# Performance work log

Measured on AMD Instinct MI355X. Metric: run time of the kernel, lower is better.

Reference implementation:

```python
import jax, jax.numpy as jnp
import numpy as np

EBIT = 8  # exponent word length -> exponent clamped to [-128, 127]
BITS = 8  # wl_activate


def block_quantize(data, bits):
    # push magnitudes away from zero (zeros map to +1e-10), as in the torch code
    data = jnp.where(data >= 0, jnp.maximum(data, 1e-10), jnp.minimum(data, -1e-10))
    # small_block='None' with dim<=4 -> single global max exponent
    max_entry = jnp.max(jnp.abs(data))
    max_exponent = jnp.clip(jnp.floor(jnp.log2(max_entry)),
                            -2.0 ** (EBIT - 1), 2.0 ** (EBIT - 1) - 1)
    i = jnp.round(data * jnp.exp2(-max_exponent + (bits - 2)))  # nearest (half-to-even, same as torch.round)
    i = jnp.clip(i, -2.0 ** (bits - 1), 2.0 ** (bits - 1) - 1)
    return i * jnp.exp2(max_exponent - (bits - 2))


def setup_inputs() -> dict:
    key = jax.random.key(0)
    x = jax.random.normal(key, (16, 2048, 4096), dtype=jnp.float32)
    return {"x": x}


def reference(x):
    return block_quantize(x, BITS)
```

## Files before the change

### kernel.cpp

```cpp
#include <hip/hip_runtime.h>
#include <math.h>

__global__ __launch_bounds__(256) void bq_max_kernel(
    const float4* __restrict__ x, unsigned int* __restrict__ max_bits,
    long long n4, const float* __restrict__ x_scalar, long long n) {
    float m = 0.0f;
    long long stride = (long long)gridDim.x * blockDim.x;
    for (long long i = (long long)blockIdx.x * blockDim.x + threadIdx.x;
         i < n4; i += stride) {
        float4 v = x[i];
        m = fmaxf(m, fmaxf(fmaxf(fabsf(v.x), fabsf(v.y)),
                           fmaxf(fabsf(v.z), fabsf(v.w))));
    }
    if (blockIdx.x == 0 && threadIdx.x == 0) {
        for (long long i = n4 * 4; i < n; ++i) m = fmaxf(m, fabsf(x_scalar[i]));
    }
    #pragma unroll
    for (int off = 32; off > 0; off >>= 1)
        m = fmaxf(m, __shfl_down(m, off, 64));
    __shared__ float smem[4];
    int lane = threadIdx.x & 63;
    int wave = threadIdx.x >> 6;
    if (lane == 0) smem[wave] = m;
    __syncthreads();
    if (threadIdx.x == 0) {
        float bm = fmaxf(fmaxf(smem[0], smem[1]), fmaxf(smem[2], smem[3]));
        bm = fmaxf(bm, 1e-10f);
        atomicMax(max_bits, __float_as_uint(bm));
    }
}

__device__ __forceinline__ float bq_one(float x, float s, float inv) {
    float d = (x >= 0.0f) ? fmaxf(x, 1e-10f) : fminf(x, -1e-10f);
    float i = rintf(d * s);
    i = fminf(fmaxf(i, -128.0f), 127.0f);
    return i * inv;
}

__global__ __launch_bounds__(256) void bq_quant_kernel(
    const float4* __restrict__ x, float4* __restrict__ out,
    const unsigned int* __restrict__ max_bits, long long n4,
    const float* __restrict__ x_scalar, float* __restrict__ out_scalar,
    long long n) {
    float max_entry = __uint_as_float(*max_bits);
    float me = (float)ilogbf(max_entry);
    me = fminf(fmaxf(me, -128.0f), 127.0f);
    float s   = exp2f(6.0f - me);
    float inv = exp2f(me - 6.0f);

    long long stride = (long long)gridDim.x * blockDim.x;
    for (long long i = (long long)blockIdx.x * blockDim.x + threadIdx.x;
         i < n4; i += stride) {
        float4 v = x[i];
        float4 r;
        r.x = bq_one(v.x, s, inv);
        r.y = bq_one(v.y, s, inv);
        r.z = bq_one(v.z, s, inv);
        r.w = bq_one(v.w, s, inv);
        out[i] = r;
    }
    if (blockIdx.x == 0 && threadIdx.x == 0) {
        for (long long i = n4 * 4; i < n; ++i)
            out_scalar[i] = bq_one(x_scalar[i], s, inv);
    }
}

extern "C" void kernel_launch(void* const* d_in, const int* in_sizes, int n_in,
                              void* d_out, int out_size, void* d_ws, size_t ws_size,
                              hipStream_t stream) {
    const float* x = (const float*)d_in[0];
    float* out = (float*)d_out;
    long long n = (long long)in_sizes[0];
    long long n4 = n / 4;
    unsigned int* max_bits = (unsigned int*)d_ws;

    hipMemsetAsync(max_bits, 0, sizeof(unsigned int), stream);

    const int block = 256;
    const int grid = 2048;
    bq_max_kernel<<<grid, block, 0, stream>>>(
        (const float4*)x, max_bits, n4, x, n);
    bq_quant_kernel<<<grid, block, 0, stream>>>(
        (const float4*)x, (float4*)out, max_bits, n4, x, out, n);
}
```

Before: 954.2 us.

## Replace atomic max with per-block partials, reverse quant loop, nontemporal stores

The max kernel now writes one partial maximum per block, and every quant block re-reduces the 2048 partials. This removes the memset launch and the global atomic. The quant loop walks its grid-stride iterations in reverse so the most recently read tail of x may still be in cache from the max pass. Output writes use nontemporal stores to keep the output from polluting the cache. Each quant block now pays for a small redundant reduction, and correctness assumes the grid stays exactly 2048 blocks.

```diff
diff --git a/kernel.cpp b/kernel.cpp
--- a/kernel.cpp
+++ b/kernel.cpp
@@ -1,8 +1,13 @@
 #include <hip/hip_runtime.h>
 #include <math.h>
 
-__global__ __launch_bounds__(256) void bq_max_kernel(
-    const float4* __restrict__ x, unsigned int* __restrict__ max_bits,
+#define GRID 2048
+#define BLOCK 256
+
+typedef float nfloat4 __attribute__((ext_vector_type(4)));
+
+__global__ __launch_bounds__(BLOCK) void bq_max_kernel(
+    const float4* __restrict__ x, float* __restrict__ partials,
     long long n4, const float* __restrict__ x_scalar, long long n) {
     float m = 0.0f;
     long long stride = (long long)gridDim.x * blockDim.x;
@@ -18,15 +23,14 @@
     #pragma unroll
     for (int off = 32; off > 0; off >>= 1)
         m = fmaxf(m, __shfl_down(m, off, 64));
-    __shared__ float smem[4];
+    __shared__ float smem[BLOCK / 64];
     int lane = threadIdx.x & 63;
     int wave = threadIdx.x >> 6;
     if (lane == 0) smem[wave] = m;
     __syncthreads();
     if (threadIdx.x == 0) {
         float bm = fmaxf(fmaxf(smem[0], smem[1]), fmaxf(smem[2], smem[3]));
-        bm = fmaxf(bm, 1e-10f);
-        atomicMax(max_bits, __float_as_uint(bm));
+        partials[blockIdx.x] = bm;
     }
 }
 
@@ -37,27 +41,47 @@
     return i * inv;
 }
 
-__global__ __launch_bounds__(256) void bq_quant_kernel(
-    const float4* __restrict__ x, float4* __restrict__ out,
-    const unsigned int* __restrict__ max_bits, long long n4,
+__global__ __launch_bounds__(BLOCK) void bq_quant_kernel(
+    const float4* __restrict__ x, nfloat4* __restrict__ out,
+    const float* __restrict__ partials, long long n4,
     const float* __restrict__ x_scalar, float* __restrict__ out_scalar,
     long long n) {
-    float max_entry = __uint_as_float(*max_bits);
-    float me = (float)ilogbf(max_entry);
-    me = fminf(fmaxf(me, -128.0f), 127.0f);
-    float s   = exp2f(6.0f - me);
-    float inv = exp2f(me - 6.0f);
+    float m = 0.0f;
+    #pragma unroll
+    for (int k = 0; k < GRID / BLOCK; ++k)
+        m = fmaxf(m, partials[threadIdx.x + k * BLOCK]);
+    #pragma unroll
+    for (int off = 32; off > 0; off >>= 1)
+        m = fmaxf(m, __shfl_down(m, off, 64));
+    __shared__ float smem[BLOCK / 64];
+    __shared__ float sc[2];
+    int lane = threadIdx.x & 63;
+    int wave = threadIdx.x >> 6;
+    if (lane == 0) smem[wave] = m;
+    __syncthreads();
+    if (threadIdx.x == 0) {
+        float bm = fmaxf(fmaxf(smem[0], smem[1]), fmaxf(smem[2], smem[3]));
+        bm = fmaxf(bm, 1e-10f);
+        int me = ilogbf(bm);
+        me = me < -128 ? -128 : (me > 127 ? 127 : me);
+        sc[0] = ldexpf(1.0f, 6 - me);
+        sc[1] = ldexpf(1.0f, me - 6);
+    }
+    __syncthreads();
+    float s = sc[0], inv = sc[1];
 
     long long stride = (long long)gridDim.x * blockDim.x;
-    for (long long i = (long long)blockIdx.x * blockDim.x + threadIdx.x;
-         i < n4; i += stride) {
+    long long base = (long long)blockIdx.x * blockDim.x + threadIdx.x;
+    long long iters = (n4 - base + stride - 1) / stride;
+    for (long long it = iters - 1; it >= 0; --it) {
+        long long i = base + it * stride;
         float4 v = x[i];
-        float4 r;
+        nfloat4 r;
         r.x = bq_one(v.x, s, inv);
         r.y = bq_one(v.y, s, inv);
         r.z = bq_one(v.z, s, inv);
         r.w = bq_one(v.w, s, inv);
-        out[i] = r;
+        __builtin_nontemporal_store(r, &out[i]);
     }
     if (blockIdx.x == 0 && threadIdx.x == 0) {
         for (long long i = n4 * 4; i < n; ++i)
@@ -72,14 +96,10 @@
     float* out = (float*)d_out;
     long long n = (long long)in_sizes[0];
     long long n4 = n / 4;
-    unsigned int* max_bits = (unsigned int*)d_ws;
+    float* partials = (float*)d_ws;
 
-    hipMemsetAsync(max_bits, 0, sizeof(unsigned int), stream);
-
-    const int block = 256;
-    const int grid = 2048;
-    bq_max_kernel<<<grid, block, 0, stream>>>(
-        (const float4*)x, max_bits, n4, x, n);
-    bq_quant_kernel<<<grid, block, 0, stream>>>(
-        (const float4*)x, (float4*)out, max_bits, n4, x, out, n);
+    bq_max_kernel<<<GRID, BLOCK, 0, stream>>>(
+        (const float4*)x, partials, n4, x, n);
+    bq_quant_kernel<<<GRID, BLOCK, 0, stream>>>(
+        (const float4*)x, (nfloat4*)out, partials, n4, x, out, n);
 }
```

After: 937.0 us. About the same (-1.8%).
